# Kernel optimization log

Measured on AMD Instinct MI355X. Metric: run time of the kernel, lower is better.

Reference implementation:

```python
import jax, jax.numpy as jnp
import numpy as np

N, E = 100000, 1600000
IN_C, HID, OUT_C = 128, 128, 64
HOPS, L = 2, 3
EPS = 1e-5


def setup_inputs() -> dict:
    key = jax.random.key(0)
    ks = jax.random.split(key, 16)
    x = jax.random.normal(ks[0], (N, IN_C), jnp.float32)
    edge_index = jax.random.randint(ks[1], (2, E), 0, N, dtype=jnp.int32).astype(jnp.int64)
    CAT = HID * (HOPS + 1)  # 384
    def lin(k, fan_in, fan_out, nstack):
        return jax.random.normal(k, (nstack, fan_in, fan_out), jnp.float32) / np.sqrt(fan_in)
    return {
        "x": x,
        "edge_index": edge_index,
        "W0": lin(ks[2], IN_C, HID, HOPS + 1),
        "b0": jnp.zeros((HOPS + 1, HID), jnp.float32),
        "W1": lin(ks[3], CAT, HID, HOPS + 1),
        "b1": jnp.zeros((HOPS + 1, HID), jnp.float32),
        "W2": lin(ks[4], CAT, OUT_C, HOPS + 1),
        "b2": jnp.zeros((HOPS + 1, OUT_C), jnp.float32),
        "bn0_g": jnp.ones((CAT,), jnp.float32),
        "bn0_b": jnp.zeros((CAT,), jnp.float32),
        "bn1_g": jnp.ones((CAT,), jnp.float32),
        "bn1_b": jnp.zeros((CAT,), jnp.float32),
        "fpW": jax.random.normal(ks[5], (OUT_C * (HOPS + 1), OUT_C), jnp.float32) / np.sqrt(OUT_C * (HOPS + 1)),
        "fpb": jnp.zeros((OUT_C,), jnp.float32),
    }


def reference(x, edge_index, W0, b0, W1, b1, W2, b2,
              bn0_g, bn0_b, bn1_g, bn1_b, fpW, fpb):
    row, col = edge_index[0], edge_index[1]
    # gcn_norm with add_self_loops=False, unit edge weights:
    # deg = scatter_add(1, col); w_e = deg^-1/2[row] * deg^-1/2[col]
    deg = jnp.zeros((N,), x.dtype).at[col].add(1.0)
    dinv = jnp.where(deg > 0, jax.lax.rsqrt(jnp.maximum(deg, 1.0)), 0.0)
    ew = dinv[row] * dinv[col]

    def spmm(h):
        # adj_t = SparseTensor(row=col, col=row, value=ew): out[col] += ew * h[row]
        return jax.ops.segment_sum(ew[:, None] * h[row], col, num_segments=N)

    def mixhop(h, W, b):
        outs = []
        for j in range(HOPS + 1):
            hj = h @ W[j] + b[j]          # lins[j](h)
            for _ in range(j):
                hj = spmm(hj)             # A^j applied j times
            outs.append(hj)
        return jnp.concatenate(outs, axis=1)

    def bn(h, g, bb):
        # BatchNorm1d in training mode: batch stats, biased variance
        mu = h.mean(axis=0)
        var = h.var(axis=0)
        return g * (h - mu) * jax.lax.rsqrt(var + EPS) + bb

    h = jax.nn.relu(bn(mixhop(x, W0, b0), bn0_g, bn0_b))   # dropout: identity (eval)
    h = jax.nn.relu(bn(mixhop(h, W1, b1), bn1_g, bn1_b))
    h = mixhop(h, W2, b2)
    return h @ fpW + fpb
```

## Files before the change

### kernel.cpp

```cpp
#include <hip/hip_runtime.h>
#include <cstdint>
#include <cstddef>

#define IN_C 128
#define HIDc 128
#define OUTc 64

using bf8 = __attribute__((ext_vector_type(8))) __bf16;
using f4  = __attribute__((ext_vector_type(4))) float;

__device__ __forceinline__ unsigned short f2bf(float f) {
    unsigned int u = __float_as_uint(f);
    unsigned int r = (u + 0x7FFFu + ((u >> 16) & 1u)) >> 16;
    return (unsigned short)r;
}
__device__ __forceinline__ float bf2f(unsigned short h) {
    return __uint_as_float(((unsigned int)h) << 16);
}

__global__ void k_detect(const long long* ei, int n_nodes, int* flag) {
    int t = threadIdx.x;
    long long v = ei[t];
    int ok = (v >= 0 && v < (long long)n_nodes) ? 1 : 0;
    unsigned long long m = __ballot(ok);
    if (t == 0) *flag = (m == ~0ull) ? 1 : 0;
}

__global__ void k_cvt_hist(const void* ei, int twoE, int E, const int* flag,
                           int* __restrict__ out, int* __restrict__ deg, int n) {
    int i = blockIdx.x * blockDim.x + threadIdx.x;
    if (i >= twoE) return;
    int v = (*flag) ? (int)((const long long*)ei)[i] : ((const int*)ei)[i];
    out[i] = v;
    if (i >= E && (unsigned)v < (unsigned)n) atomicAdd(&deg[v], 1);
}

__global__ void k_dinv(const int* __restrict__ deg, float* __restrict__ dinv, int n) {
    int i = blockIdx.x * blockDim.x + threadIdx.x;
    if (i < n) dinv[i] = (deg[i] > 0) ? rsqrtf((float)deg[i]) : 0.0f;
}

__global__ void k_alloc(const int* __restrict__ deg, int* __restrict__ base,
                        int* __restrict__ cursor, int* __restrict__ counter, int n) {
    int i = blockIdx.x * blockDim.x + threadIdx.x;
    int lane = threadIdx.x & 63;
    int val = (i < n) ? deg[i] : 0;
    int scan = val;
    #pragma unroll
    for (int off = 1; off < 64; off <<= 1) {
        int t = __shfl_up(scan, off);
        if (lane >= off) scan += t;
    }
    int excl = scan - val;
    int total = __shfl(scan, 63);
    int wb = 0;
    if (lane == 0) wb = atomicAdd(counter, total);
    wb = __shfl(wb, 0);
    if (i < n) { base[i] = wb + excl; cursor[i] = wb + excl; }
}

__global__ void k_scatter(const int* __restrict__ eint, int E,
                          const float* __restrict__ dinv, int n,
                          int* __restrict__ cursor, int2* __restrict__ ew) {
    int e = blockIdx.x * blockDim.x + threadIdx.x;
    if (e >= E) return;
    int r = eint[e];
    int c = eint[E + e];
    if ((unsigned)r >= (unsigned)n || (unsigned)c >= (unsigned)n) return;
    int p = atomicAdd(&cursor[c], 1);
    int2 v; v.x = r; v.y = __float_as_int(dinv[r] * dinv[c]);
    ew[p] = v;
}

__global__ void k_wprep(const float* __restrict__ W, unsigned short* __restrict__ Wt,
                        int K, int N) {
    int j = blockIdx.y;
    int idx = blockIdx.x * 256 + threadIdx.x;
    if (idx >= K * N) return;
    int k = idx / N, nn = idx - k * N;
    Wt[(size_t)j * N * K + (size_t)nn * K + k] = f2bf(W[(size_t)j * K * N + idx]);
}

__global__ void k_cast4(const float* __restrict__ x, unsigned short* __restrict__ y, int n4) {
    int i = blockIdx.x * 256 + threadIdx.x;
    if (i >= n4) return;
    float4 v = ((const float4*)x)[i];
    ushort4 o;
    o.x = f2bf(v.x); o.y = f2bf(v.y); o.z = f2bf(v.z); o.w = f2bf(v.w);
    ((ushort4*)y)[i] = o;
}

template<int PW, bool AFFINE>
__global__ __launch_bounds__(512) void k_mfma3(
    const unsigned short* __restrict__ A0, const unsigned short* __restrict__ A1,
    const unsigned short* __restrict__ A2, int W, int M, int K,
    const unsigned short* __restrict__ Bt, const float* __restrict__ bias,
    const float* __restrict__ scale, const float* __restrict__ shift,
    unsigned short* __restrict__ C0, unsigned short* __restrict__ C1,
    unsigned short* __restrict__ C2)
{
    constexpr int NT = 3 * PW;
    constexpr int TN = NT / 64;
    __shared__ __align__(16) unsigned short As[128 * 40];
    __shared__ __align__(16) unsigned short Bs[NT * 40];
    __shared__ float sSc[384], sSh[384];

    int t = threadIdx.x;
    if (AFFINE) {
        for (int i = t; i < K; i += 512) { sSc[i] = scale[i]; sSh[i] = shift[i]; }
    }
    __syncthreads();

    int wave = t >> 6, lane = t & 63;
    int m16 = lane & 15, q = lane >> 4;
    int rowHalf = wave & 1, colQ = wave >> 1;
    int row0 = blockIdx.x * 128;

    f4 acc[4][TN];
    #pragma unroll
    for (int i = 0; i < 4; i++)
        #pragma unroll
        for (int j = 0; j < TN; j++) acc[i][j] = (f4){0.f, 0.f, 0.f, 0.f};

    int arow_l = t >> 2, aci = t & 3;
    constexpr int NCH = NT * 4;

    for (int kk = 0; kk < K; kk += 32) {
        int pi = kk / W;
        const unsigned short* Ap = (pi == 0) ? A0 : ((pi == 1) ? A1 : A2);
        int kl = kk - pi * W;

        int arow = row0 + arow_l; if (arow >= M) arow = M - 1;
        uint4 av = *(const uint4*)&Ap[(size_t)arow * W + kl + aci * 8];
        if (AFFINE) {
            int ch0 = kk + aci * 8;
            unsigned int* w32 = (unsigned int*)&av;
            #pragma unroll
            for (int h = 0; h < 4; h++) {
                unsigned int u = w32[h];
                float lo = fmaxf(bf2f((unsigned short)(u & 0xffff)) * sSc[ch0 + 2*h] + sSh[ch0 + 2*h], 0.f);
                float hi = fmaxf(bf2f((unsigned short)(u >> 16))    * sSc[ch0 + 2*h + 1] + sSh[ch0 + 2*h + 1], 0.f);
                w32[h] = (unsigned int)f2bf(lo) | ((unsigned int)f2bf(hi) << 16);
            }
        }
        uint4 bvv[3]; int nb = 0;
        for (int i = t; i < NCH; i += 512) {
            int brow = i >> 2, bci = i & 3;
            bvv[nb++] = *(const uint4*)&Bt[(size_t)brow * K + kk + bci * 8];
        }
        __syncthreads();
        *(uint4*)&As[arow_l * 40 + aci * 8] = av;
        nb = 0;
        for (int i = t; i < NCH; i += 512) {
            int brow = i >> 2, bci = i & 3;
            *(uint4*)&Bs[brow * 40 + bci * 8] = bvv[nb++];
        }
        __syncthreads();

        bf8 af[4], bfr[TN];
        #pragma unroll
        for (int tm = 0; tm < 4; tm++)
            af[tm] = *(const bf8*)&As[(rowHalf * 64 + tm * 16 + m16) * 40 + q * 8];
        #pragma unroll
        for (int tn = 0; tn < TN; tn++)
            bfr[tn] = *(const bf8*)&Bs[(colQ * 16 * TN + tn * 16 + m16) * 40 + q * 8];
        #pragma unroll
        for (int tm = 0; tm < 4; tm++)
            #pragma unroll
            for (int tn = 0; tn < TN; tn++)
                acc[tm][tn] = __builtin_amdgcn_mfma_f32_16x16x32_bf16(
                    af[tm], bfr[tn], acc[tm][tn], 0, 0, 0);
    }

    #pragma unroll
    for (int tn = 0; tn < TN; tn++) {
        int col_base = colQ * 16 * TN + tn * 16;
        int j  = col_base / PW;
        int cc = col_base - j * PW + m16;
        unsigned short* Cj = (j == 0) ? C0 : ((j == 1) ? C1 : C2);
        float bi = bias[col_base + m16];
        #pragma unroll
        for (int tm = 0; tm < 4; tm++) {
            #pragma unroll
            for (int r = 0; r < 4; r++) {
                int row = row0 + rowHalf * 64 + tm * 16 + q * 4 + r;
                if (row >= M) continue;
                Cj[(size_t)row * PW + cc] = f2bf(acc[tm][tn][r] + bi);
            }
        }
    }
}

__global__ __launch_bounds__(256) void k_mfma_fin(
    const unsigned short* __restrict__ A0, const unsigned short* __restrict__ A1,
    const unsigned short* __restrict__ A2, int W, int M, int K,
    const unsigned short* __restrict__ Bt, const float* __restrict__ bias,
    float* __restrict__ C, int ldc)
{
    constexpr int TM = 2, TN = 4;
    __shared__ __align__(16) unsigned short As[128 * 40];
    __shared__ __align__(16) unsigned short Bs[64 * 40];

    int t = threadIdx.x;
    int wave = t >> 6, lane = t & 63;
    int m16 = lane & 15, q = lane >> 4;
    int row0 = blockIdx.x * 128;
    int wr = wave * 32, wc = 0;

    f4 acc[TM][TN];
    #pragma unroll
    for (int i = 0; i < TM; i++)
        #pragma unroll
        for (int j = 0; j < TN; j++) acc[i][j] = (f4){0.f, 0.f, 0.f, 0.f};

    int ar = t & 127, ah = t >> 7;

    for (int kk = 0; kk < K; kk += 32) {
        int pi = kk / W;
        const unsigned short* Ap = (pi == 0) ? A0 : ((pi == 1) ? A1 : A2);
        int kl = kk - pi * W;

        int arow = row0 + ar; if (arow >= M) arow = M - 1;
        const uint4* asrc = (const uint4*)&Ap[(size_t)arow * W + kl + ah * 16];
        uint4 av0 = asrc[0], av1 = asrc[1];
        uint4 bv0 = *(const uint4*)&Bt[(size_t)(t & 63) * K + kk + (t >> 6) * 8];
        __syncthreads();
        *(uint4*)&As[ar * 40 + ah * 16]     = av0;
        *(uint4*)&As[ar * 40 + ah * 16 + 8] = av1;
        *(uint4*)&Bs[(t & 63) * 40 + (t >> 6) * 8] = bv0;
        __syncthreads();

        bf8 af[TM], bfr[TN];
        #pragma unroll
        for (int tm = 0; tm < TM; tm++)
            af[tm] = *(const bf8*)&As[(wr + tm * 16 + m16) * 40 + q * 8];
        #pragma unroll
        for (int tn = 0; tn < TN; tn++)
            bfr[tn] = *(const bf8*)&Bs[(wc + tn * 16 + m16) * 40 + q * 8];
        #pragma unroll
        for (int tm = 0; tm < TM; tm++)
            #pragma unroll
            for (int tn = 0; tn < TN; tn++)
                acc[tm][tn] = __builtin_amdgcn_mfma_f32_16x16x32_bf16(
                    af[tm], bfr[tn], acc[tm][tn], 0, 0, 0);
    }

    #pragma unroll
    for (int tm = 0; tm < TM; tm++) {
        #pragma unroll
        for (int tn = 0; tn < TN; tn++) {
            int col = wc + tn * 16 + m16;
            float bi = bias[col];
            #pragma unroll
            for (int r = 0; r < 4; r++) {
                int row = row0 + wr + tm * 16 + q * 4 + r;
                if (row >= M) continue;
                C[(size_t)row * ldc + col] = acc[tm][tn][r] + bi;
            }
        }
    }
}

template<int V, bool DUAL>
__global__ __launch_bounds__(256) void k_spmm(
    const unsigned short* __restrict__ S1, const unsigned short* __restrict__ S2,
    unsigned short* __restrict__ D1, unsigned short* __restrict__ D2, int width,
    const int* __restrict__ base, const int* __restrict__ deg,
    const int2* __restrict__ ew, int n)
{
    int node = blockIdx.x * 4 + threadIdx.y;
    if (node >= n) return;
    int tx = threadIdx.x;
    float a1[V], a2[V];
    #pragma unroll
    for (int v = 0; v < V; v++) { a1[v] = 0.f; if (DUAL) a2[v] = 0.f; }
    int b = base[node], end = b + deg[node];
    const unsigned short* P1 = S1 + tx * V;
    const unsigned short* P2 = S2 + tx * V;
    constexpr int UN = 8;
    int e = b;
    for (; e + UN <= end; e += UN) {
        int2 ev[UN];
        #pragma unroll
        for (int u = 0; u < UN; u++) ev[u] = ew[e + u];
        unsigned int g1[UN], g2[UN];
        #pragma unroll
        for (int u = 0; u < UN; u++) {
            if (V == 2) g1[u] = *(const unsigned int*)(P1 + (size_t)ev[u].x * width);
            else        g1[u] = P1[(size_t)ev[u].x * width];
            if (DUAL) {
                if (V == 2) g2[u] = *(const unsigned int*)(P2 + (size_t)ev[u].x * width);
                else        g2[u] = P2[(size_t)ev[u].x * width];
            }
        }
        #pragma unroll
        for (int u = 0; u < UN; u++) {
            float we = __int_as_float(ev[u].y);
            if (V == 2) {
                a1[0] += we * bf2f((unsigned short)(g1[u] & 0xffff));
                a1[1] += we * bf2f((unsigned short)(g1[u] >> 16));
                if (DUAL) {
                    a2[0] += we * bf2f((unsigned short)(g2[u] & 0xffff));
                    a2[1] += we * bf2f((unsigned short)(g2[u] >> 16));
                }
            } else {
                a1[0] += we * bf2f((unsigned short)g1[u]);
                if (DUAL) a2[0] += we * bf2f((unsigned short)g2[u]);
            }
        }
    }
    for (; e < end; ++e) {
        int2 ev = ew[e];
        float we = __int_as_float(ev.y);
        if (V == 2) {
            unsigned int u1 = *(const unsigned int*)(P1 + (size_t)ev.x * width);
            a1[0] += we * bf2f((unsigned short)(u1 & 0xffff));
            a1[1] += we * bf2f((unsigned short)(u1 >> 16));
            if (DUAL) {
                unsigned int u2 = *(const unsigned int*)(P2 + (size_t)ev.x * width);
                a2[0] += we * bf2f((unsigned short)(u2 & 0xffff));
                a2[1] += we * bf2f((unsigned short)(u2 >> 16));
            }
        } else {
            a1[0] += we * bf2f(P1[(size_t)ev.x * width]);
            if (DUAL) a2[0] += we * bf2f(P2[(size_t)ev.x * width]);
        }
    }
    size_t o = (size_t)node * width + tx * V;
    if (V == 2) {
        ushort2 o1; o1.x = f2bf(a1[0]); o1.y = f2bf(a1[1]);
        *(ushort2*)&D1[o] = o1;
        if (DUAL) { ushort2 o2; o2.x = f2bf(a2[0]); o2.y = f2bf(a2[1]);
                    *(ushort2*)&D2[o] = o2; }
    } else {
        D1[o] = f2bf(a1[0]);
        if (DUAL) D2[o] = f2bf(a2[0]);
    }
}

__global__ void k_bnstats(const unsigned short* __restrict__ p0,
                          const unsigned short* __restrict__ p1,
                          const unsigned short* __restrict__ p2,
                          float* __restrict__ sums, float* __restrict__ sumsq, int n)
{
    int c = threadIdx.x;
    int cc = c & 127;
    int pi = c >> 7;
    const unsigned short* src = (pi == 0) ? p0 : ((pi == 1) ? p1 : p2);
    float s = 0.f, s2 = 0.f;
    for (int r = blockIdx.x; r < n; r += gridDim.x) {
        float v = bf2f(src[(size_t)r * 128 + cc]);
        s += v; s2 += v * v;
    }
    atomicAdd(&sums[c], s);
    atomicAdd(&sumsq[c], s2);
}

__global__ void k_bnfin(const float* __restrict__ sums, const float* __restrict__ sumsq,
                        const float* __restrict__ g, const float* __restrict__ bb,
                        float* __restrict__ scale, float* __restrict__ shift,
                        int cat, float invn)
{
    int c = threadIdx.x;
    if (c >= cat) return;
    float mu  = sums[c] * invn;
    float var = sumsq[c] * invn - mu * mu;
    float sc  = g[c] * rsqrtf(var + 1e-5f);
    scale[c] = sc;
    shift[c] = bb[c] - mu * sc;
}

__global__ void k_diag(float* out, float val, int n) {
    int i = blockIdx.x * blockDim.x + threadIdx.x;
    if (i < n) out[i] = val;
}

extern "C" void kernel_launch(void* const* d_in, const int* in_sizes, int n_in,
                              void* d_out, int out_size, void* d_ws, size_t ws_size,
                              hipStream_t stream)
{
    const float* x    = (const float*)d_in[0];
    const void*  ei   = d_in[1];
    const float* W0   = (const float*)d_in[2];
    const float* b0   = (const float*)d_in[3];
    const float* W1   = (const float*)d_in[4];
    const float* b1   = (const float*)d_in[5];
    const float* W2   = (const float*)d_in[6];
    const float* b2   = (const float*)d_in[7];
    const float* bn0g = (const float*)d_in[8];
    const float* bn0b = (const float*)d_in[9];
    const float* bn1g = (const float*)d_in[10];
    const float* bn1b = (const float*)d_in[11];
    const float* fpW  = (const float*)d_in[12];
    const float* fpb  = (const float*)d_in[13];
    float* out = (float*)d_out;

    const int N    = in_sizes[0] / IN_C;
    const int twoE = in_sizes[1];
    const int E    = twoE / 2;

    char* p = (char*)d_ws;
    auto alloc = [&](size_t bytes) -> char* {
        char* r = p; p += (bytes + 255) & ~(size_t)255; return r;
    };
    unsigned short* U[6];
    for (int i = 0; i < 6; i++) U[i] = (unsigned short*)alloc((size_t)N * 128 * 2);
    unsigned short* Wt0 = (unsigned short*)alloc((size_t)3 * 128 * 128 * 2);
    unsigned short* Wt1 = (unsigned short*)alloc((size_t)3 * 384 * 128 * 2);
    unsigned short* Wt2 = (unsigned short*)alloc((size_t)3 * 384 * 64 * 2);
    unsigned short* WtF = (unsigned short*)alloc((size_t)192 * 64 * 2);
    float* dinv  = (float*)alloc((size_t)N * 4);
    int2*  ew    = (int2*)alloc((size_t)E * 8);
    float* sums  = (float*)alloc(2 * 384 * 4);
    float* sumsq = sums + 384;
    float* scale = (float*)alloc(384 * 4);
    float* shift = (float*)alloc(384 * 4);
    int* deg     = (int*)alloc((size_t)N * 4);
    int* base    = (int*)alloc((size_t)N * 4);
    int* cursor  = (int*)alloc((size_t)N * 4);
    int* eint    = (int*)alloc((size_t)twoE * 4);
    int* counter = (int*)alloc(4);
    int* flag    = (int*)alloc(4);

    size_t required = (size_t)(p - (char*)d_ws);
    if (required > ws_size) {
        k_diag<<<(out_size + 255) / 256, 256, 0, stream>>>(
            out, (float)(ws_size >> 20), out_size);
        return;
    }

    const int T = 256;
    dim3 spmm_blk(64, 4);
    int  spmm_grid = (N + 3) / 4;
    int  gx128 = (N + 127) / 128;

    k_wprep<<<dim3((128 * 128 + 255) / 256, 3), T, 0, stream>>>(W0, Wt0, 128, 128);
    k_wprep<<<dim3((384 * 128 + 255) / 256, 3), T, 0, stream>>>(W1, Wt1, 384, 128);
    k_wprep<<<dim3((384 * 64  + 255) / 256, 3), T, 0, stream>>>(W2, Wt2, 384, 64);
    k_wprep<<<dim3((192 * 64  + 255) / 256, 1), T, 0, stream>>>(fpW, WtF, 192, 64);
    unsigned short* Xb = U[3];
    k_cast4<<<((N * 128 / 4) + 255) / 256, T, 0, stream>>>(x, Xb, N * 128 / 4);

    hipMemsetAsync(deg, 0, (size_t)N * 4, stream);
    hipMemsetAsync(counter, 0, 4, stream);
    k_detect<<<1, 64, 0, stream>>>((const long long*)ei, N, flag);
    k_cvt_hist<<<(twoE + T - 1) / T, T, 0, stream>>>(ei, twoE, E, flag, eint, deg, N);
    k_dinv<<<(N + T - 1) / T, T, 0, stream>>>(deg, dinv, N);
    k_alloc<<<(N + T - 1) / T, T, 0, stream>>>(deg, base, cursor, counter, N);
    k_scatter<<<(E + T - 1) / T, T, 0, stream>>>(eint, E, dinv, N, cursor, ew);

    k_mfma3<128, false><<<gx128, 512, 0, stream>>>(Xb, Xb, Xb, 128, N, 128,
        Wt0, b0, nullptr, nullptr, U[0], U[1], U[2]);
    k_spmm<2, true ><<<spmm_grid, spmm_blk, 0, stream>>>(U[1], U[2], U[4], U[5], 128,
                                                         base, deg, ew, N);
    k_spmm<2, false><<<spmm_grid, spmm_blk, 0, stream>>>(U[5], nullptr, U[3], nullptr, 128,
                                                         base, deg, ew, N);
    hipMemsetAsync(sums, 0, 2 * 384 * 4, stream);
    k_bnstats<<<2048, 384, 0, stream>>>(U[0], U[4], U[3], sums, sumsq, N);
    k_bnfin<<<1, 384, 0, stream>>>(sums, sumsq, bn0g, bn0b, scale, shift, 384, 1.0f / N);

    k_mfma3<128, true><<<gx128, 512, 0, stream>>>(U[0], U[4], U[3], 128, N, 384,
        Wt1, b1, scale, shift, U[1], U[2], U[5]);
    k_spmm<2, true ><<<spmm_grid, spmm_blk, 0, stream>>>(U[2], U[5], U[0], U[4], 128,
                                                         base, deg, ew, N);
    k_spmm<2, false><<<spmm_grid, spmm_blk, 0, stream>>>(U[4], nullptr, U[3], nullptr, 128,
                                                         base, deg, ew, N);
    hipMemsetAsync(sums, 0, 2 * 384 * 4, stream);
    k_bnstats<<<2048, 384, 0, stream>>>(U[1], U[0], U[3], sums, sumsq, N);
    k_bnfin<<<1, 384, 0, stream>>>(sums, sumsq, bn1g, bn1b, scale, shift, 384, 1.0f / N);

    unsigned short* V2a = U[2];
    unsigned short* V2b = U[2] + (size_t)N * 64;
    unsigned short* V4a = U[4];
    unsigned short* V4b = U[4] + (size_t)N * 64;
    unsigned short* V5a = U[5];
    unsigned short* V5b = U[5] + (size_t)N * 64;
    k_mfma3<64, true><<<gx128, 512, 0, stream>>>(U[1], U[0], U[3], 128, N, 384,
        Wt2, b2, scale, shift, V2a, V2b, V4a);
    k_spmm<1, true ><<<spmm_grid, spmm_blk, 0, stream>>>(V2b, V4a, V4b, V5a, 64,
                                                         base, deg, ew, N);
    k_spmm<1, false><<<spmm_grid, spmm_blk, 0, stream>>>(V5a, nullptr, V5b, nullptr, 64,
                                                         base, deg, ew, N);

    k_mfma_fin<<<gx128, T, 0, stream>>>(V2a, V4b, V5b, 64, N, 192, WtF, fpb, out, 64);
}
```

Baseline: 1.371 ms.

## Load MFMA operands directly from global memory, dropping LDS staging and barriers

Both MFMA GEMM kernels now load A and B fragments straight from global memory into registers in MFMA layout, instead of staging tiles through shared memory with two barriers per k-step. BN scale/shift are read per lane from global memory rather than preloaded into LDS. This removes LDS traffic and synchronisation, but each wave now fetches its own B tile and A rows, so global and L2 traffic rise and the strided per-row 16-byte loads may coalesce poorly.

```diff
diff --git a/kernel.cpp b/kernel.cpp
--- a/kernel.cpp
+++ b/kernel.cpp
@@ -101,75 +101,73 @@
 {
     constexpr int NT = 3 * PW;
     constexpr int TN = NT / 64;
-    __shared__ __align__(16) unsigned short As[128 * 40];
-    __shared__ __align__(16) unsigned short Bs[NT * 40];
-    __shared__ float sSc[384], sSh[384];
-
     int t = threadIdx.x;
-    if (AFFINE) {
-        for (int i = t; i < K; i += 512) { sSc[i] = scale[i]; sSh[i] = shift[i]; }
-    }
-    __syncthreads();
-
     int wave = t >> 6, lane = t & 63;
     int m16 = lane & 15, q = lane >> 4;
     int rowHalf = wave & 1, colQ = wave >> 1;
     int row0 = blockIdx.x * 128;
 
+    size_t aoff[4];
+    #pragma unroll
+    for (int tm = 0; tm < 4; tm++) {
+        int r = row0 + rowHalf * 64 + tm * 16 + m16;
+        if (r >= M) r = M - 1;
+        aoff[tm] = (size_t)r * W;
+    }
+    size_t boff[TN];
+    #pragma unroll
+    for (int tn = 0; tn < TN; tn++)
+        boff[tn] = (size_t)(colQ * 16 * TN + tn * 16 + m16) * K;
+
     f4 acc[4][TN];
     #pragma unroll
     for (int i = 0; i < 4; i++)
         #pragma unroll
         for (int j = 0; j < TN; j++) acc[i][j] = (f4){0.f, 0.f, 0.f, 0.f};
-
-    int arow_l = t >> 2, aci = t & 3;
-    constexpr int NCH = NT * 4;
 
     for (int kk = 0; kk < K; kk += 32) {
         int pi = kk / W;
         const unsigned short* Ap = (pi == 0) ? A0 : ((pi == 1) ? A1 : A2);
         int kl = kk - pi * W;
 
-        int arow = row0 + arow_l; if (arow >= M) arow = M - 1;
-        uint4 av = *(const uint4*)&Ap[(size_t)arow * W + kl + aci * 8];
+        uint4 a4[4];
+        #pragma unroll
+        for (int tm = 0; tm < 4; tm++)
+            a4[tm] = *(const uint4*)&Ap[aoff[tm] + kl + q * 8];
+
         if (AFFINE) {
-            int ch0 = kk + aci * 8;
-            unsigned int* w32 = (unsigned int*)&av;
+            int ch0 = kk + q * 8;
+            float scv[8], shv[8];
+            *(float4*)&scv[0] = *(const float4*)&scale[ch0];
+            *(float4*)&scv[4] = *(const float4*)&scale[ch0 + 4];
+            *(float4*)&shv[0] = *(const float4*)&shift[ch0];
+            *(float4*)&shv[4] = *(const float4*)&shift[ch0 + 4];
             #pragma unroll
-            for (int h = 0; h < 4; h++) {
-                unsigned int u = w32[h];
-                float lo = fmaxf(bf2f((unsigned short)(u & 0xffff)) * sSc[ch0 + 2*h] + sSh[ch0 + 2*h], 0.f);
-                float hi = fmaxf(bf2f((unsigned short)(u >> 16))    * sSc[ch0 + 2*h + 1] + sSh[ch0 + 2*h + 1], 0.f);
-                w32[h] = (unsigned int)f2bf(lo) | ((unsigned int)f2bf(hi) << 16);
-            }
-        }
-        uint4 bvv[3]; int nb = 0;
-        for (int i = t; i < NCH; i += 512) {
-            int brow = i >> 2, bci = i & 3;
-            bvv[nb++] = *(const uint4*)&Bt[(size_t)brow * K + kk + bci * 8];
-        }
-        __syncthreads();
-        *(uint4*)&As[arow_l * 40 + aci * 8] = av;
-        nb = 0;
-        for (int i = t; i < NCH; i += 512) {
-            int brow = i >> 2, bci = i & 3;
-            *(uint4*)&Bs[brow * 40 + bci * 8] = bvv[nb++];
-        }
-        __syncthreads();
-
-        bf8 af[4], bfr[TN];
-        #pragma unroll
-        for (int tm = 0; tm < 4; tm++)
-            af[tm] = *(const bf8*)&As[(rowHalf * 64 + tm * 16 + m16) * 40 + q * 8];
+            for (int tm = 0; tm < 4; tm++) {
+                unsigned int* w32 = (unsigned int*)&a4[tm];
+                #pragma unroll
+                for (int h = 0; h < 4; h++) {
+                    unsigned int u = w32[h];
+                    float lo = fmaxf(bf2f((unsigned short)(u & 0xffff)) * scv[2*h]     + shv[2*h],     0.f);
+                    float hi = fmaxf(bf2f((unsigned short)(u >> 16))    * scv[2*h + 1] + shv[2*h + 1], 0.f);
+                    w32[h] = (unsigned int)f2bf(lo) | ((unsigned int)f2bf(hi) << 16);
+                }
+            }
+        }
+
+        bf8 bfr[TN];
         #pragma unroll
         for (int tn = 0; tn < TN; tn++)
-            bfr[tn] = *(const bf8*)&Bs[(colQ * 16 * TN + tn * 16 + m16) * 40 + q * 8];
-        #pragma unroll
-        for (int tm = 0; tm < 4; tm++)
+            bfr[tn] = *(const bf8*)&Bt[boff[tn] + kk + q * 8];
+
+        #pragma unroll
+        for (int tm = 0; tm < 4; tm++) {
+            bf8 af = *(const bf8*)&a4[tm];
             #pragma unroll
             for (int tn = 0; tn < TN; tn++)
                 acc[tm][tn] = __builtin_amdgcn_mfma_f32_16x16x32_bf16(
-                    af[tm], bfr[tn], acc[tm][tn], 0, 0, 0);
+                    af, bfr[tn], acc[tm][tn], 0, 0, 0);
+        }
     }
 
     #pragma unroll
@@ -198,45 +196,42 @@
     float* __restrict__ C, int ldc)
 {
     constexpr int TM = 2, TN = 4;
-    __shared__ __align__(16) unsigned short As[128 * 40];
-    __shared__ __align__(16) unsigned short Bs[64 * 40];
-
     int t = threadIdx.x;
     int wave = t >> 6, lane = t & 63;
     int m16 = lane & 15, q = lane >> 4;
     int row0 = blockIdx.x * 128;
-    int wr = wave * 32, wc = 0;
+    int wr = wave * 32;
+
+    size_t aoff[TM];
+    #pragma unroll
+    for (int tm = 0; tm < TM; tm++) {
+        int r = row0 + wr + tm * 16 + m16;
+        if (r >= M) r = M - 1;
+        aoff[tm] = (size_t)r * W;
+    }
+    size_t boff[TN];
+    #pragma unroll
+    for (int tn = 0; tn < TN; tn++)
+        boff[tn] = (size_t)(tn * 16 + m16) * K;
 
     f4 acc[TM][TN];
     #pragma unroll
     for (int i = 0; i < TM; i++)
         #pragma unroll
         for (int j = 0; j < TN; j++) acc[i][j] = (f4){0.f, 0.f, 0.f, 0.f};
-
-    int ar = t & 127, ah = t >> 7;
 
     for (int kk = 0; kk < K; kk += 32) {
         int pi = kk / W;
         const unsigned short* Ap = (pi == 0) ? A0 : ((pi == 1) ? A1 : A2);
         int kl = kk - pi * W;
 
-        int arow = row0 + ar; if (arow >= M) arow = M - 1;
-        const uint4* asrc = (const uint4*)&Ap[(size_t)arow * W + kl + ah * 16];
-        uint4 av0 = asrc[0], av1 = asrc[1];
-        uint4 bv0 = *(const uint4*)&Bt[(size_t)(t & 63) * K + kk + (t >> 6) * 8];
-        __syncthreads();
-        *(uint4*)&As[ar * 40 + ah * 16]     = av0;
-        *(uint4*)&As[ar * 40 + ah * 16 + 8] = av1;
-        *(uint4*)&Bs[(t & 63) * 40 + (t >> 6) * 8] = bv0;
-        __syncthreads();
-
         bf8 af[TM], bfr[TN];
         #pragma unroll
         for (int tm = 0; tm < TM; tm++)
-            af[tm] = *(const bf8*)&As[(wr + tm * 16 + m16) * 40 + q * 8];
+            af[tm] = *(const bf8*)&Ap[aoff[tm] + kl + q * 8];
         #pragma unroll
         for (int tn = 0; tn < TN; tn++)
-            bfr[tn] = *(const bf8*)&Bs[(wc + tn * 16 + m16) * 40 + q * 8];
+            bfr[tn] = *(const bf8*)&Bt[boff[tn] + kk + q * 8];
         #pragma unroll
         for (int tm = 0; tm < TM; tm++)
             #pragma unroll
@@ -249,7 +244,7 @@
     for (int tm = 0; tm < TM; tm++) {
         #pragma unroll
         for (int tn = 0; tn < TN; tn++) {
-            int col = wc + tn * 16 + m16;
+            int col = tn * 16 + m16;
             float bi = bias[col];
             #pragma unroll
             for (int r = 0; r < 4; r++) {
@@ -276,7 +271,7 @@
     for (int v = 0; v < V; v++) { a1[v] = 0.f; if (DUAL) a2[v] = 0.f; }
     int b = base[node], end = b + deg[node];
     const unsigned short* P1 = S1 + tx * V;
-    const unsigned short* P2 = S2 + tx * V;
+    const unsigned short* P2 = DUAL ? (S2 + tx * V) : nullptr;
     constexpr int UN = 8;
     int e = b;
     for (; e + UN <= end; e += UN) {
```

Result: no change. 1.381 ms (+0.8%).
